# Optimization experiments

Hardware: AMD Instinct MI355X
Metric: run time of the kernel (lower is better)

## Reference

```python
import jax, jax.numpy as jnp
import numpy as np

B, T, C, H = 32, 1024, 384, 64

def setup_inputs() -> dict:
    key = jax.random.key(0)
    k1, k2, k3, k4 = jax.random.split(key, 4)
    x = jax.random.normal(k1, (B, T, C), dtype=jnp.float32)
    s = 1.0 / np.sqrt(C)
    Wk = jax.random.normal(k2, (C, H), dtype=jnp.float32) * s
    Wq = jax.random.normal(k3, (C, H), dtype=jnp.float32) * s
    Wv = jax.random.normal(k4, (C, H), dtype=jnp.float32) * s
    return {"x": x, "Wk": Wk, "Wq": Wq, "Wv": Wv}

def reference(x, Wk, Wq, Wv):
    # Single-head causal attention (dropout = identity, eval mode).
    Tn = x.shape[1]
    k = jnp.einsum('btc,ch->bth', x, Wk)   # [B,T,H]
    q = jnp.einsum('btc,ch->bth', x, Wq)
    v = jnp.einsum('btc,ch->bth', x, Wv)
    scale = k.shape[-1] ** -0.5
    wei = jnp.einsum('bth,bsh->bts', q, k) * scale  # [B,T,T]
    causal = jnp.tril(jnp.ones((Tn, Tn), dtype=bool))
    wei = jnp.where(causal, wei, -jnp.inf)
    wei = jax.nn.softmax(wei, axis=-1)
    out = jnp.einsum('bts,bsh->bth', wei, v)  # [B,T,H]
    return out
```

## Files before the change

### kernel.cpp

```cpp
#include <hip/hip_runtime.h>

#define BB 32
#define TT 1024
#define CCH 384
#define HH 64

typedef short short8 __attribute__((ext_vector_type(8)));
typedef float f32x4 __attribute__((ext_vector_type(4)));
typedef unsigned short ushort;

static __device__ __forceinline__ ushort f2bf(float f) {
    union { float f; unsigned u; } v; v.f = f;
    unsigned r = v.u + 0x7fff + ((v.u >> 16) & 1);
    return (ushort)(r >> 16);
}

__global__ void wswz(const float* __restrict__ Wk, const float* __restrict__ Wq,
                     const float* __restrict__ Wv, ushort* __restrict__ wf) {
    const int mat = blockIdx.x, ks = blockIdx.y;
    const float* W = (mat == 0) ? Wk : ((mat == 1) ? Wq : Wv);
    const int t = threadIdx.x;
    const int ct = t >> 6, lane = t & 63, quad = lane >> 4, l15 = lane & 15;
    const int col = ct * 16 + l15;
    short8 d;
#pragma unroll
    for (int j = 0; j < 8; ++j)
        d[j] = (short)f2bf(W[(ks * 32 + quad * 8 + j) * 64 + col]);
    *(short8*)(wf + (((mat * 12 + ks) * 4 + ct) << 9) + lane * 8) = d;
}

#define XSTR 388
#define VS_STRIDE 68

__global__ __launch_bounds__(256, 2) void qkv(const float* __restrict__ x,
                                              const ushort* __restrict__ wf,
                                              ushort* __restrict__ kb,
                                              ushort* __restrict__ qb,
                                              ushort* __restrict__ vtb) {
    const int r0 = blockIdx.x * 64;
    const int tid = threadIdx.x;
    const int wv = tid >> 6, lane = tid & 63, l15 = lane & 15, quad = lane >> 4;

    __shared__ ushort xs[64 * XSTR];

#pragma unroll
    for (int kb3 = 0; kb3 < 3; ++kb3) {
        const int kbase = kb3 * 128;
        const int seg = (tid & 7) * 16;
#pragma unroll
        for (int i = 0; i < 2; ++i) {
            const int r = (tid >> 3) + 32 * i;
            const float* src = x + (size_t)(r0 + r) * CCH + kbase + seg;
            f32x4 v0 = *(const f32x4*)(src);
            f32x4 v1 = *(const f32x4*)(src + 4);
            f32x4 v2 = *(const f32x4*)(src + 8);
            f32x4 v3 = *(const f32x4*)(src + 12);
            short8 p0, p1;
#pragma unroll
            for (int j = 0; j < 4; ++j) {
                p0[j]     = (short)f2bf(v0[j]);
                p0[j + 4] = (short)f2bf(v1[j]);
                p1[j]     = (short)f2bf(v2[j]);
                p1[j + 4] = (short)f2bf(v3[j]);
            }
            *(short8*)(xs + r * XSTR + kbase + seg) = p0;
            *(short8*)(xs + r * XSTR + kbase + seg + 8) = p1;
        }
    }
    __syncthreads();

    f32x4 acc[12] = {};
    short8 bf[2][12];
#pragma unroll
    for (int m = 0; m < 3; ++m)
#pragma unroll
        for (int ct = 0; ct < 4; ++ct)
            bf[0][m * 4 + ct] = *(const short8*)(wf + (((m * 12 + 0) * 4 + ct) << 9) + lane * 8);

#pragma unroll
    for (int ks = 0; ks < 12; ++ks) {
        short8 a = *(const short8*)(xs + (wv * 16 + l15) * XSTR + ks * 32 + quad * 8);
        if (ks < 11) {
#pragma unroll
            for (int m = 0; m < 3; ++m)
#pragma unroll
                for (int ct = 0; ct < 4; ++ct)
                    bf[(ks + 1) & 1][m * 4 + ct] =
                        *(const short8*)(wf + (((m * 12 + ks + 1) * 4 + ct) << 9) + lane * 8);
        }
#pragma unroll
        for (int f = 0; f < 12; ++f)
            acc[f] = __builtin_amdgcn_mfma_f32_16x16x32_bf16(a, bf[ks & 1][f], acc[f], 0, 0, 0);
    }

#pragma unroll
    for (int ct = 0; ct < 4; ++ct) {
#pragma unroll
        for (int r = 0; r < 4; ++r) {
            int row = r0 + wv * 16 + quad * 4 + r;
            int col = ct * 16 + l15;
            kb[row * 64 + col] = f2bf(acc[0 + ct][r]);
            qb[row * 64 + col] = f2bf(acc[4 + ct][r]);
        }
    }
    __syncthreads();
    ushort* vs = xs;
#pragma unroll
    for (int ct = 0; ct < 4; ++ct)
#pragma unroll
        for (int r = 0; r < 4; ++r)
            vs[(wv * 16 + quad * 4 + r) * VS_STRIDE + ct * 16 + l15] = f2bf(acc[8 + ct][r]);
    __syncthreads();
    {
        const int col = tid >> 2;
        const int rbase = (tid & 3) * 16;
        short8 d0, d1;
#pragma unroll
        for (int j = 0; j < 8; ++j) {
            d0[j] = (short)vs[(rbase + j) * VS_STRIDE + col];
            d1[j] = (short)vs[(rbase + 8 + j) * VS_STRIDE + col];
        }
        const int b = r0 >> 10;
        const int t = (r0 & 1023) + rbase;
        *(short8*)(vtb + b * 65536 + col * 1024 + t) = d0;
        *(short8*)(vtb + b * 65536 + col * 1024 + t + 8) = d1;
    }
}

#define PSTR2 40
#define KSTR 72
#define VSTR 136

__global__ __launch_bounds__(256, 2) void attn(const ushort* __restrict__ qb,
                                               const ushort* __restrict__ kb,
                                               const ushort* __restrict__ vtb,
                                               float* __restrict__ out) {
    const int y = blockIdx.y;
    const int qt = (y < 8) ? (15 - y) : (y - 8);
    const int b = blockIdx.x;
    const int t0 = qt * 64;
    const int tid = threadIdx.x;
    const int w = tid >> 6, lane = tid & 63, l15 = lane & 15, quad = lane >> 4;

    __shared__ __align__(16) char arena[56320];
    ushort* Ks = (ushort*)arena;
    ushort* Vs = (ushort*)(arena + 18432);
    ushort* Ps = (ushort*)(arena + 35840);
    ushort* Psw = Ps + w * 64 * PSTR2;

    const ushort* kbb = kb  + (size_t)b * 65536;
    const ushort* vbb = vtb + (size_t)b * 65536;

    short8 qf0[4], qf1[4];
#pragma unroll
    for (int m = 0; m < 4; ++m) {
        const int qrow = b * 1024 + t0 + m * 16 + l15;
        qf0[m] = *(const short8*)(qb + qrow * 64 + quad * 8);
        qf1[m] = *(const short8*)(qb + qrow * 64 + 32 + quad * 8);
    }

    f32x4 o[4][4] = {};
    float li[4][4] = {};
    const float c1 = 0.125f * 1.4426950408889634f;
    const float c2 = 10.0f * 1.4426950408889634f;

    const int nst = (qt >> 1) + 1;

    short8 kr[4], vr[4];
#pragma unroll
    for (int i = 0; i < 4; ++i) {
        int c = tid + i * 256;
        kr[i] = *(const short8*)(kbb + (c >> 3) * 64 + (c & 7) * 8);
        vr[i] = *(const short8*)(vbb + (c >> 4) * 1024 + (c & 15) * 8);
    }

    for (int it = 0; it < nst; ++it) {
        const int s0 = it * 128;
        __syncthreads();
#pragma unroll
        for (int i = 0; i < 4; ++i) {
            int c = tid + i * 256;
            *(short8*)(Ks + (c >> 3) * KSTR + (c & 7) * 8) = kr[i];
            *(short8*)(Vs + (c >> 4) * VSTR + (c & 15) * 8) = vr[i];
        }
        __syncthreads();
        if (it + 1 < nst) {
            const int sn = s0 + 128;
#pragma unroll
            for (int i = 0; i < 4; ++i) {
                int c = tid + i * 256;
                kr[i] = *(const short8*)(kbb + (sn + (c >> 3)) * 64 + (c & 7) * 8);
                vr[i] = *(const short8*)(vbb + (c >> 4) * 1024 + sn + (c & 15) * 8);
            }
        }

        f32x4 s[4][2];
        __builtin_amdgcn_s_setprio(1);
#pragma unroll
        for (int g = 0; g < 2; ++g) {
            const ushort* kp = Ks + (w * 32 + g * 16 + l15) * KSTR + quad * 8;
            short8 b0 = *(const short8*)(kp);
            short8 b1 = *(const short8*)(kp + 32);
#pragma unroll
            for (int m = 0; m < 4; ++m) {
                f32x4 z = {};
                z = __builtin_amdgcn_mfma_f32_16x16x32_bf16(qf0[m], b0, z, 0, 0, 0);
                s[m][g] = __builtin_amdgcn_mfma_f32_16x16x32_bf16(qf1[m], b1, z, 0, 0, 0);
            }
        }
        __builtin_amdgcn_s_setprio(0);

        if (it + 1 < nst) {
#pragma unroll
            for (int m = 0; m < 4; ++m)
#pragma unroll
                for (int g = 0; g < 2; ++g)
#pragma unroll
                    for (int r = 0; r < 4; ++r) {
                        float p = exp2f(s[m][g][r] * c1 - c2);
                        li[m][r] += p;
                        Psw[(m * 16 + quad * 4 + r) * PSTR2 + g * 16 + l15] = f2bf(p);
                    }
        } else {
#pragma unroll
            for (int m = 0; m < 4; ++m)
#pragma unroll
                for (int g = 0; g < 2; ++g)
#pragma unroll
                    for (int r = 0; r < 4; ++r) {
                        const int trow = t0 + m * 16 + quad * 4 + r;
                        const int col = s0 + w * 32 + g * 16 + l15;
                        float p = (col <= trow) ? exp2f(s[m][g][r] * c1 - c2) : 0.f;
                        li[m][r] += p;
                        Psw[(m * 16 + quad * 4 + r) * PSTR2 + g * 16 + l15] = f2bf(p);
                    }
        }

        short8 pa[4];
#pragma unroll
        for (int m = 0; m < 4; ++m)
            pa[m] = *(const short8*)(Psw + (m * 16 + l15) * PSTR2 + quad * 8);

        __builtin_amdgcn_s_setprio(1);
        short8 vbf[4];
#pragma unroll
        for (int ct = 0; ct < 4; ++ct)
            vbf[ct] = *(const short8*)(Vs + (ct * 16 + l15) * VSTR + w * 32 + quad * 8);
#pragma unroll
        for (int m = 0; m < 4; ++m)
#pragma unroll
            for (int ct = 0; ct < 4; ++ct)
                o[m][ct] = __builtin_amdgcn_mfma_f32_16x16x32_bf16(pa[m], vbf[ct], o[m][ct], 0, 0, 0);
        __builtin_amdgcn_s_setprio(0);
    }

    __syncthreads();

#pragma unroll
    for (int m = 0; m < 4; ++m)
#pragma unroll
        for (int r = 0; r < 4; ++r) {
            float rs = li[m][r];
#pragma unroll
            for (int off = 1; off < 16; off <<= 1)
                rs += __shfl_xor(rs, off);
            li[m][r] = rs;
        }

    f32x4 ow[4] = {};
    float lw[4] = {};
#pragma unroll
    for (int m = 0; m < 4; ++m)
        if (m == w) {
#pragma unroll
            for (int ct = 0; ct < 4; ++ct) ow[ct] = o[m][ct];
#pragma unroll
            for (int r = 0; r < 4; ++r) lw[r] = li[m][r];
        }

    float* cmbO = (float*)arena;
    float* cmbL = (float*)(arena + 52224);
#pragma unroll
    for (int m = 0; m < 4; ++m)
        if (m != w) {
            const int slot = w * 3 + m - (m > w ? 1 : 0);
            float* dst = cmbO + slot * 1088;
#pragma unroll
            for (int ct = 0; ct < 4; ++ct)
#pragma unroll
                for (int r = 0; r < 4; ++r)
                    dst[ct * 272 + (quad * 4 + r) * 17 + l15] = o[m][ct][r];
            if (l15 == 0)
#pragma unroll
                for (int r = 0; r < 4; ++r)
                    cmbL[(w * 4 + m) * 16 + quad * 4 + r] = li[m][r];
        }
    __syncthreads();
#pragma unroll
    for (int wp = 0; wp < 4; ++wp)
        if (wp != w) {
            const int slot = wp * 3 + w - (w > wp ? 1 : 0);
            const float* src = cmbO + slot * 1088;
#pragma unroll
            for (int ct = 0; ct < 4; ++ct)
#pragma unroll
                for (int r = 0; r < 4; ++r)
                    ow[ct][r] += src[ct * 272 + (quad * 4 + r) * 17 + l15];
#pragma unroll
            for (int r = 0; r < 4; ++r)
                lw[r] += cmbL[(wp * 4 + w) * 16 + quad * 4 + r];
        }

#pragma unroll
    for (int r = 0; r < 4; ++r) {
        float inv = 1.0f / lw[r];
        int t = t0 + w * 16 + quad * 4 + r;
#pragma unroll
        for (int ct = 0; ct < 4; ++ct)
            out[b * 65536 + t * 64 + ct * 16 + l15] = ow[ct][r] * inv;
    }
}

extern "C" void kernel_launch(void* const* d_in, const int* in_sizes, int n_in,
                              void* d_out, int out_size, void* d_ws, size_t ws_size,
                              hipStream_t stream) {
    const float* x  = (const float*)d_in[0];
    const float* Wk = (const float*)d_in[1];
    const float* Wq = (const float*)d_in[2];
    const float* Wv = (const float*)d_in[3];

    char* ws = (char*)d_ws;
    ushort* wf  = (ushort*)ws;
    ushort* kb  = (ushort*)(ws + 256 * 1024);
    ushort* qb  = (ushort*)(ws + 256 * 1024 + 4u * 1024 * 1024);
    ushort* vtb = (ushort*)(ws + 256 * 1024 + 8u * 1024 * 1024);

    wswz<<<dim3(3, 12), dim3(256), 0, stream>>>(Wk, Wq, Wv, wf);
    qkv<<<dim3(512), dim3(256), 0, stream>>>(x, wf, kb, qb, vtb);
    attn<<<dim3(32, 16), dim3(256), 0, stream>>>(qb, kb, vtb, (float*)d_out);
}
```

Before: 121.9 us.

## Halve attention query tile to 32 rows, doubling blocks and raising occupancy

Each attention block now handles 32 query rows instead of 64, so the grid doubles to 32x32. Launch bounds rise to 3 blocks per CU, helped by the smaller shared-memory arena. The cross-warp combine is rewritten so every warp writes its partial O and row-sum to shared memory, and each warp then reduces one row-block/column-half slice for the output. This is meant to give better load balance across CUs for the causal triangle and more latency hiding, at the cost of loading each K/V tile twice as often overall.

```diff
diff --git a/kernel.cpp b/kernel.cpp
--- a/kernel.cpp
+++ b/kernel.cpp
@@ -131,40 +131,44 @@
 #define KSTR 72
 #define VSTR 136
 
-__global__ __launch_bounds__(256, 2) void attn(const ushort* __restrict__ qb,
+__global__ __launch_bounds__(256, 3) void attn(const ushort* __restrict__ qb,
                                                const ushort* __restrict__ kb,
                                                const ushort* __restrict__ vtb,
                                                float* __restrict__ out) {
     const int y = blockIdx.y;
-    const int qt = (y < 8) ? (15 - y) : (y - 8);
+    int qt;
+    if (y < 8)       qt = 31 - y;
+    else if (y < 16) qt = y - 8;
+    else if (y < 24) qt = 39 - y;
+    else             qt = y - 16;
     const int b = blockIdx.x;
-    const int t0 = qt * 64;
+    const int t0 = qt * 32;
     const int tid = threadIdx.x;
     const int w = tid >> 6, lane = tid & 63, l15 = lane & 15, quad = lane >> 4;
 
-    __shared__ __align__(16) char arena[56320];
+    __shared__ __align__(16) char arena[46080];
     ushort* Ks = (ushort*)arena;
     ushort* Vs = (ushort*)(arena + 18432);
     ushort* Ps = (ushort*)(arena + 35840);
-    ushort* Psw = Ps + w * 64 * PSTR2;
+    ushort* Psw = Ps + w * 32 * PSTR2;
 
     const ushort* kbb = kb  + (size_t)b * 65536;
     const ushort* vbb = vtb + (size_t)b * 65536;
 
-    short8 qf0[4], qf1[4];
-#pragma unroll
-    for (int m = 0; m < 4; ++m) {
+    short8 qf0[2], qf1[2];
+#pragma unroll
+    for (int m = 0; m < 2; ++m) {
         const int qrow = b * 1024 + t0 + m * 16 + l15;
         qf0[m] = *(const short8*)(qb + qrow * 64 + quad * 8);
         qf1[m] = *(const short8*)(qb + qrow * 64 + 32 + quad * 8);
     }
 
-    f32x4 o[4][4] = {};
-    float li[4][4] = {};
+    f32x4 o[2][4] = {};
+    float li[2][4] = {};
     const float c1 = 0.125f * 1.4426950408889634f;
     const float c2 = 10.0f * 1.4426950408889634f;
 
-    const int nst = (qt >> 1) + 1;
+    const int nst = (qt >> 2) + 1;
 
     short8 kr[4], vr[4];
 #pragma unroll
@@ -194,7 +198,7 @@
             }
         }
 
-        f32x4 s[4][2];
+        f32x4 s[2][2];
         __builtin_amdgcn_s_setprio(1);
 #pragma unroll
         for (int g = 0; g < 2; ++g) {
@@ -202,7 +206,7 @@
             short8 b0 = *(const short8*)(kp);
             short8 b1 = *(const short8*)(kp + 32);
 #pragma unroll
-            for (int m = 0; m < 4; ++m) {
+            for (int m = 0; m < 2; ++m) {
                 f32x4 z = {};
                 z = __builtin_amdgcn_mfma_f32_16x16x32_bf16(qf0[m], b0, z, 0, 0, 0);
                 s[m][g] = __builtin_amdgcn_mfma_f32_16x16x32_bf16(qf1[m], b1, z, 0, 0, 0);
@@ -212,7 +216,7 @@
 
         if (it + 1 < nst) {
 #pragma unroll
-            for (int m = 0; m < 4; ++m)
+            for (int m = 0; m < 2; ++m)
 #pragma unroll
                 for (int g = 0; g < 2; ++g)
 #pragma unroll
@@ -223,7 +227,7 @@
                     }
         } else {
 #pragma unroll
-            for (int m = 0; m < 4; ++m)
+            for (int m = 0; m < 2; ++m)
 #pragma unroll
                 for (int g = 0; g < 2; ++g)
 #pragma unroll
@@ -236,9 +240,9 @@
                     }
         }
 
-        short8 pa[4];
-#pragma unroll
-        for (int m = 0; m < 4; ++m)
+        short8 pa[2];
+#pragma unroll
+        for (int m = 0; m < 2; ++m)
             pa[m] = *(const short8*)(Psw + (m * 16 + l15) * PSTR2 + quad * 8);
 
         __builtin_amdgcn_s_setprio(1);
@@ -247,7 +251,7 @@
         for (int ct = 0; ct < 4; ++ct)
             vbf[ct] = *(const short8*)(Vs + (ct * 16 + l15) * VSTR + w * 32 + quad * 8);
 #pragma unroll
-        for (int m = 0; m < 4; ++m)
+        for (int m = 0; m < 2; ++m)
 #pragma unroll
             for (int ct = 0; ct < 4; ++ct)
                 o[m][ct] = __builtin_amdgcn_mfma_f32_16x16x32_bf16(pa[m], vbf[ct], o[m][ct], 0, 0, 0);
@@ -257,7 +261,7 @@
     __syncthreads();
 
 #pragma unroll
-    for (int m = 0; m < 4; ++m)
+    for (int m = 0; m < 2; ++m)
 #pragma unroll
         for (int r = 0; r < 4; ++r) {
             float rs = li[m][r];
@@ -267,57 +271,43 @@
             li[m][r] = rs;
         }
 
-    f32x4 ow[4] = {};
-    float lw[4] = {};
-#pragma unroll
-    for (int m = 0; m < 4; ++m)
-        if (m == w) {
-#pragma unroll
-            for (int ct = 0; ct < 4; ++ct) ow[ct] = o[m][ct];
-#pragma unroll
-            for (int r = 0; r < 4; ++r) lw[r] = li[m][r];
-        }
-
-    float* cmbO = (float*)arena;
-    float* cmbL = (float*)(arena + 52224);
-#pragma unroll
-    for (int m = 0; m < 4; ++m)
-        if (m != w) {
-            const int slot = w * 3 + m - (m > w ? 1 : 0);
-            float* dst = cmbO + slot * 1088;
-#pragma unroll
-            for (int ct = 0; ct < 4; ++ct)
-#pragma unroll
-                for (int r = 0; r < 4; ++r)
-                    dst[ct * 272 + (quad * 4 + r) * 17 + l15] = o[m][ct][r];
-            if (l15 == 0)
-#pragma unroll
-                for (int r = 0; r < 4; ++r)
-                    cmbL[(w * 4 + m) * 16 + quad * 4 + r] = li[m][r];
-        }
-    __syncthreads();
-#pragma unroll
-    for (int wp = 0; wp < 4; ++wp)
-        if (wp != w) {
-            const int slot = wp * 3 + w - (w > wp ? 1 : 0);
-            const float* src = cmbO + slot * 1088;
-#pragma unroll
-            for (int ct = 0; ct < 4; ++ct)
-#pragma unroll
-                for (int r = 0; r < 4; ++r)
-                    ow[ct][r] += src[ct * 272 + (quad * 4 + r) * 17 + l15];
+    float* slotO = (float*)arena;
+    float* slotL = (float*)(arena + 34816);
+#pragma unroll
+    for (int m = 0; m < 2; ++m) {
+        const int sl = w * 2 + m;
+#pragma unroll
+        for (int ct = 0; ct < 4; ++ct)
 #pragma unroll
             for (int r = 0; r < 4; ++r)
-                lw[r] += cmbL[(wp * 4 + w) * 16 + quad * 4 + r];
-        }
-
-#pragma unroll
-    for (int r = 0; r < 4; ++r) {
-        float inv = 1.0f / lw[r];
-        int t = t0 + w * 16 + quad * 4 + r;
-#pragma unroll
-        for (int ct = 0; ct < 4; ++ct)
-            out[b * 65536 + t * 64 + ct * 16 + l15] = ow[ct][r] * inv;
+                slotO[(sl * 4 + ct) * 272 + (quad * 4 + r) * 17 + l15] = o[m][ct][r];
+        if (l15 == 0)
+#pragma unroll
+            for (int r = 0; r < 4; ++r)
+                slotL[sl * 16 + quad * 4 + r] = li[m][r];
+    }
+    __syncthreads();
+
+    {
+        const int mh = w >> 1, cb = (w & 1) * 2;
+#pragma unroll
+        for (int r = 0; r < 4; ++r) {
+            float lsum = 0.f;
+#pragma unroll
+            for (int wp = 0; wp < 4; ++wp)
+                lsum += slotL[(wp * 2 + mh) * 16 + quad * 4 + r];
+            const float inv = 1.0f / lsum;
+            const int t = t0 + mh * 16 + quad * 4 + r;
+#pragma unroll
+            for (int cc = 0; cc < 2; ++cc) {
+                const int ct = cb + cc;
+                float v = 0.f;
+#pragma unroll
+                for (int wp = 0; wp < 4; ++wp)
+                    v += slotO[((wp * 2 + mh) * 4 + ct) * 272 + (quad * 4 + r) * 17 + l15];
+                out[b * 65536 + t * 64 + ct * 16 + l15] = v * inv;
+            }
+        }
     }
 }
 
@@ -337,5 +327,5 @@
 
     wswz<<<dim3(3, 12), dim3(256), 0, stream>>>(Wk, Wq, Wv, wf);
     qkv<<<dim3(512), dim3(256), 0, stream>>>(x, wf, kb, qb, vtb);
-    attn<<<dim3(32, 16), dim3(256), 0, stream>>>(qb, kb, vtb, (float*)d_out);
-}
+    attn<<<dim3(32, 32), dim3(256), 0, stream>>>(qb, kb, vtb, (float*)d_out);
+}
```

Measured after the change: 121.0 us. No clear change (-0.7%).
